# Performance work log

Hardware: AMD Instinct MI355X
Metric: run time of the kernel (lower is better)

Reference implementation:

```python
import jax, jax.numpy as jnp
import numpy as np

LEAN_TAU = 0.25
LEAN_DELTA = 0.35
O_ID = 0
NUM_LABELS = 9
HIDDEN = 1024


def setup_inputs() -> dict:
    key = jax.random.key(0)
    k = jax.random.split(key, 7)
    B, T = 64, 512
    hidden_states = jax.random.normal(k[0], (B, T, HIDDEN), dtype=jnp.float32)
    attention_mask = jnp.ones((B, T), dtype=jnp.int32)
    labels = jax.random.randint(k[1], (B, T), 0, NUM_LABELS).astype(jnp.int64)
    emis_w = jax.random.normal(k[2], (NUM_LABELS, HIDDEN), dtype=jnp.float32) * 0.02
    emis_b = jnp.zeros((NUM_LABELS,), dtype=jnp.float32)
    start_trans = jax.random.uniform(k[3], (NUM_LABELS,), minval=-0.1, maxval=0.1)
    end_trans = jax.random.uniform(k[4], (NUM_LABELS,), minval=-0.1, maxval=0.1)
    trans = jax.random.uniform(k[5], (NUM_LABELS, NUM_LABELS), minval=-0.1, maxval=0.1)
    return {
        "hidden_states": hidden_states,
        "emis_w": emis_w,
        "emis_b": emis_b,
        "start_trans": start_trans,
        "end_trans": end_trans,
        "trans": trans,
        "attention_mask": attention_mask,
        "labels": labels,
    }


def _crf_nll(logits, tags, mask, start_trans, end_trans, trans):
    """torchcrf CRF(batch_first=True), reduction='mean': -mean(log p(tags | logits))."""
    # time-major: [T, B, ...]
    e = jnp.swapaxes(logits, 0, 1)              # [T, B, L]
    tg = jnp.swapaxes(tags, 0, 1)               # [T, B]
    mk = jnp.swapaxes(mask, 0, 1).astype(logits.dtype)  # [T, B]
    B = e.shape[1]
    bidx = jnp.arange(B)

    # ----- numerator: score of gold path -----
    score0 = start_trans[tg[0]] + e[0, bidx, tg[0]]      # [B]
    last0 = tg[0]

    def num_step(carry, xs):
        score, last = carry
        e_t, t_t, t_prev, m_t = xs
        score = score + (trans[t_prev, t_t] + e_t[bidx, t_t]) * m_t
        last = jnp.where(m_t.astype(bool), t_t, last)
        return (score, last), None

    (num, last), _ = jax.lax.scan(num_step, (score0, last0),
                                  (e[1:], tg[1:], tg[:-1], mk[1:]))
    num = num + end_trans[last]

    # ----- denominator: partition via forward algorithm -----
    alpha0 = start_trans[None, :] + e[0]                 # [B, L]

    def den_step(alpha, xs):
        e_t, m_t = xs
        # alpha[b, i] + trans[i, j] + e_t[b, j] -> logsumexp over i
        nxt = jax.nn.logsumexp(alpha[:, :, None] + trans[None, :, :] + e_t[:, None, :], axis=1)
        alpha = jnp.where(m_t[:, None].astype(bool), nxt, alpha)
        return alpha, None

    alpha, _ = jax.lax.scan(den_step, alpha0, (e[1:], mk[1:]))
    den = jax.nn.logsumexp(alpha + end_trans[None, :], axis=1)  # [B]

    llh = num - den
    return -jnp.mean(llh)


def reference(hidden_states, emis_w, emis_b, start_trans, end_trans, trans,
              attention_mask, labels):
    # emission head
    logits = jnp.einsum('bth,lh->btl', hidden_states, emis_w) + emis_b  # [B, T, L]
    # strip special tokens ([CLS]/[SEP] positions)
    logits = logits[:, 1:-1, :]
    tok_mask = attention_mask[:, 1:-1].astype(bool)

    # lean-to-O on uncertain positions (torch.no_grad -> stop_gradient)
    det = jax.lax.stop_gradient(logits)
    top2 = jax.lax.top_k(det, 2)[0]                      # [B, T-2, 2]
    uncertain = ((top2[..., 0] - top2[..., 1]) < LEAN_TAU) & tok_mask
    logits = logits.at[..., O_ID].add(uncertain.astype(logits.dtype) * LEAN_DELTA)

    gold = labels[:, 1:-1]
    tags = jnp.where(gold == -100, 0, gold)
    mask = gold != -100
    return _crf_nll(logits, tags, mask, start_trans, end_trans, trans)
```

## Files before the change

### kernel.cpp

```cpp
#include <hip/hip_runtime.h>
#include <math.h>

#define HIDDEN 1024
#define NL 9
#define LEAN_TAU 0.25f
#define LEAN_DELTA 0.35f
#define LCH 16
#define TFIX 512
#define TOKFIX 510

typedef __attribute__((ext_vector_type(8))) short short8v;
typedef __attribute__((ext_vector_type(4))) float f32x4;
typedef __attribute__((ext_vector_type(4))) unsigned uint4v;
union frag_u { uint4v u; short8v s; };

__device__ __forceinline__ unsigned pk2(float a, float b) {
  return (__float_as_uint(b) & 0xffff0000u) | (__float_as_uint(a) >> 16);
}

__global__ __launch_bounds__(256) void mfma_k(
    const float* __restrict__ hs, const float* __restrict__ w,
    const float* __restrict__ bias, const int* __restrict__ amask,
    float* __restrict__ e, int B) {
  const int nTok = B * TOKFIX;
  const int wave = threadIdx.x >> 6, lane = threadIdx.x & 63;
  const int g = lane >> 4, c = lane & 15;
  __shared__ unsigned short aw[4][16][264];
  __shared__ float4 cp[3][64];

  const int base = blockIdx.x * 16;
  {
    int b = base / TOKFIX, t = base - b * TOKFIX;
#pragma unroll
    for (int j = 0; j < 16; ++j) {
      const int tok = base + j;
      const float* src =
          hs + ((size_t)b * TFIX + ((tok < nTok) ? t : 0) + 1) * HIDDEN;
      const float4 f =
          *reinterpret_cast<const float4*>(src + wave * 256 + lane * 4);
      uint2 pk;
      pk.x = pk2(f.x, f.y);
      pk.y = pk2(f.z, f.w);
      *reinterpret_cast<uint2*>(&aw[wave][j][lane * 4]) = pk;
      if (++t >= TOKFIX) { t = 0; ++b; }
    }
  }
  frag_u bfrag[8];
  {
    const int brow = (c < NL) ? c : 0;
    const float* wp = w + (size_t)brow * HIDDEN + wave * 256 + g * 8;
#pragma unroll
    for (int s = 0; s < 8; ++s) {
      const float4 u0 = *reinterpret_cast<const float4*>(wp + s * 32);
      const float4 u1 = *reinterpret_cast<const float4*>(wp + s * 32 + 4);
      unsigned d0 = pk2(u0.x, u0.y), d1 = pk2(u0.z, u0.w);
      unsigned d2 = pk2(u1.x, u1.y), d3 = pk2(u1.z, u1.w);
      if (c >= NL) d0 = d1 = d2 = d3 = 0u;
      bfrag[s].u = uint4v{d0, d1, d2, d3};
    }
  }
  __syncthreads();

  f32x4 acc = {0.f, 0.f, 0.f, 0.f};
#pragma unroll
  for (int s = 0; s < 8; ++s) {
    const short8v a =
        *reinterpret_cast<const short8v*>(&aw[wave][c][s * 32 + g * 8]);
    acc = __builtin_amdgcn_mfma_f32_16x16x32_bf16(a, bfrag[s].s, acc, 0, 0, 0);
  }

  if (wave != 0) cp[wave - 1][lane] = *reinterpret_cast<float4*>(&acc);
  __syncthreads();
  if (wave == 0) {
#pragma unroll
    for (int k = 0; k < 3; ++k) {
      const float4 p = cp[k][lane];
      acc[0] += p.x; acc[1] += p.y; acc[2] += p.z; acc[3] += p.w;
    }
    const float bc = (c < NL) ? bias[c] : 0.f;
#pragma unroll
    for (int j = 0; j < 4; ++j) {
      const int tok = base + g * 4 + j;
      const int tokc = (tok < nTok) ? tok : 0;
      const int b = tokc / TOKFIX, t = tokc - b * TOKFIX;
      const float v = acc[j] + bc;
      float m1 = (c < NL) ? v : -1e30f, m2 = -1e30f;
#pragma unroll
      for (int off = 1; off < 16; off <<= 1) {
        const float om1 = __shfl_xor(m1, off);
        const float om2 = __shfl_xor(m2, off);
        const float hi = fmaxf(m1, om1);
        const float lo = fminf(m1, om1);
        m2 = fmaxf(lo, fmaxf(m2, om2));
        m1 = hi;
      }
      const bool unc = (m1 - m2 < LEAN_TAU) && (amask[b * TFIX + t + 1] != 0);
      const float vout = v + ((unc && c == 0) ? LEAN_DELTA : 0.f);
      if (c < NL && tok < nTok) e[(size_t)tok * NL + c] = vout;
    }
  }
}

__global__ __launch_bounds__(64) void chunk_k(
    const float* __restrict__ e, const int* __restrict__ labels,
    const float* __restrict__ trans, float* __restrict__ Pout,
    int B, int T, int C) {
  const int TOK = T - 2;
  __shared__ float e2[7][LCH][NL];
  __shared__ float tr2[NL * NL];
  __shared__ int msk[7][LCH];
  const int tid = threadIdx.x;
  const int nG = B * C;
  const int gbase = blockIdx.x * 7;

  for (int idx = tid; idx < NL * NL; idx += 64) tr2[idx] = trans[idx];
  for (int idx = tid; idx < 7 * LCH * NL; idx += 64) {
    const int sub = idx / (LCH * NL), rem = idx % (LCH * NL);
    const int step = rem / NL, j = rem % NL;
    const int g = gbase + sub;
    if (g < nG) {
      const int b = g / C, c = g % C;
      const int t = 1 + c * LCH + step;
      if (t < TOK) e2[sub][step][j] = e[((size_t)b * TOK + t) * NL + j];
    }
  }
  for (int idx = tid; idx < 7 * LCH; idx += 64) {
    const int sub = idx / LCH, step = idx % LCH;
    const int g = gbase + sub;
    if (g < nG) {
      const int b = g / C, c = g % C;
      const int t = 1 + c * LCH + step;
      msk[sub][step] = (t < TOK) ? (labels[(size_t)b * T + 1 + t] != -100) : 0;
    }
  }
  __syncthreads();

  const int sub = tid / NL, i = tid % NL;
  const int g = gbase + sub;
  const bool act = (sub < 7) && (g < nG);
  int len = 1;
  if (act) { const int c = g % C; len = min(LCH, TOK - (1 + c * LCH)); }

  float W[NL][NL];
#pragma unroll
  for (int k = 0; k < NL; ++k)
#pragma unroll
    for (int j = 0; j < NL; ++j) W[k][j] = __expf(tr2[k * NL + j]);

  float P[NL];
  {
    const int m0 = act ? msk[sub][0] : 0;
#pragma unroll
    for (int j = 0; j < NL; ++j)
      P[j] = m0 ? (tr2[i * NL + j] + e2[sub][0][j])
                : ((i == j) ? 0.f : -1e30f);
  }
  for (int step = 1; step < len; ++step) {
    const int mt = msk[sub][step];
    float mx = P[0];
#pragma unroll
    for (int k = 1; k < NL; ++k) mx = fmaxf(mx, P[k]);
    float E[NL];
#pragma unroll
    for (int k = 0; k < NL; ++k) E[k] = __expf(P[k] - mx);
    float Pn[NL];
#pragma unroll
    for (int j = 0; j < NL; ++j) {
      float s = 0.f;
#pragma unroll
      for (int k = 0; k < NL; ++k) s = fmaf(E[k], W[k][j], s);
      Pn[j] = mx + __logf(s) + e2[sub][step][j];
    }
#pragma unroll
    for (int j = 0; j < NL; ++j) P[j] = mt ? Pn[j] : P[j];
  }
  if (act) {
    float* dst = Pout + (size_t)g * 81 + i * NL;
#pragma unroll
    for (int j = 0; j < NL; ++j) dst[j] = P[j];
  }
}

__global__ __launch_bounds__(64) void combine_k(
    const float* __restrict__ e, const int* __restrict__ labels,
    const float* __restrict__ start_t, const float* __restrict__ end_t,
    const float* __restrict__ trans, const float* __restrict__ Pmat,
    float* __restrict__ llh, int B, int T, int C) {
  const int TOK = T - 2;
  const int b = blockIdx.x, lane = threadIdx.x;
  const float* eb = e + (size_t)b * TOK * NL;
  const int* lb = labels + (size_t)b * T + 1;

  const int g0r = lb[0];
  const int tg0 = (g0r == -100) ? 0 : g0r;
  float nsum = 0.f;
  int pack = -1;
  for (int t = 1 + lane; t < TOK; t += 64) {
    const int gr = lb[t], pr = lb[t - 1];
    if (gr != -100) {
      const int cur = gr;
      const int prev = (pr == -100) ? 0 : pr;
      nsum += trans[prev * NL + cur] + eb[t * NL + cur];
      pack = (t << 4) | cur;
    }
  }
#pragma unroll
  for (int off = 32; off; off >>= 1) {
    nsum += __shfl_xor(nsum, off);
    pack = max(pack, __shfl_xor(pack, off));
  }
  const int last = (pack < 0) ? tg0 : (pack & 15);
  const float num = start_t[tg0] + eb[tg0] + nsum + end_t[last];

  float alpha = (lane < NL) ? (start_t[lane] + eb[lane]) : -1e30f;
  for (int c = 0; c < C; ++c) {
    const float* Pc = Pmat + ((size_t)b * C + c) * 81;
    float col[NL];
#pragma unroll
    for (int i = 0; i < NL; ++i)
      col[i] = (lane < NL) ? Pc[i * NL + lane] : -1e30f;
    float s[NL];
    float mx = -1e30f;
#pragma unroll
    for (int i = 0; i < NL; ++i) {
      const float ai = __shfl(alpha, i);
      s[i] = ai + col[i];
      mx = fmaxf(mx, s[i]);
    }
    float sum = 0.f;
#pragma unroll
    for (int i = 0; i < NL; ++i) sum += __expf(s[i] - mx);
    const float nx = mx + __logf(sum);
    alpha = (lane < NL) ? nx : -1e30f;
  }
  const float v = (lane < NL) ? (alpha + end_t[lane]) : -1e30f;
  float mx = v;
#pragma unroll
  for (int off = 32; off; off >>= 1) mx = fmaxf(mx, __shfl_xor(mx, off));
  float sum = (lane < NL) ? __expf(v - mx) : 0.f;
#pragma unroll
  for (int off = 32; off; off >>= 1) sum += __shfl_xor(sum, off);
  const float den = mx + __logf(sum);
  if (lane == 0) llh[b] = num - den;
}

__global__ __launch_bounds__(64) void reduce_k(const float* __restrict__ llh,
                                               float* __restrict__ out, int B) {
  float v = 0.f;
  for (int i = threadIdx.x; i < B; i += 64) v += llh[i];
#pragma unroll
  for (int off = 32; off; off >>= 1) v += __shfl_xor(v, off);
  if (threadIdx.x == 0) out[0] = -v / (float)B;
}

extern "C" void kernel_launch(void* const* d_in, const int* in_sizes, int n_in,
                              void* d_out, int out_size, void* d_ws,
                              size_t ws_size, hipStream_t stream) {
  const float* hs     = (const float*)d_in[0];
  const float* w      = (const float*)d_in[1];
  const float* bias   = (const float*)d_in[2];
  const float* st     = (const float*)d_in[3];
  const float* et     = (const float*)d_in[4];
  const float* tr     = (const float*)d_in[5];
  const int*   amask  = (const int*)d_in[6];
  const int*   labels = (const int*)d_in[7];

  const int T = 512;
  const int B = in_sizes[6] / T;
  const int TOK = T - 2;
  const int C = (TOK - 1 + LCH - 1) / LCH;

  float* e    = (float*)d_ws;
  float* llh  = e + (size_t)B * TOK * NL;
  float* Pmat = llh + B;

  const int nTok = B * TOK;
  const int nTile = (nTok + 15) / 16;
  mfma_k<<<nTile, 256, 0, stream>>>(hs, w, bias, amask, e, B);
  const int nG = B * C;
  chunk_k<<<(nG + 6) / 7, 64, 0, stream>>>(e, labels, tr, Pmat, B, T, C);
  combine_k<<<B, 64, 0, stream>>>(e, labels, st, et, tr, Pmat, llh, B, T, C);
  reduce_k<<<1, 64, 0, stream>>>(llh, (float*)d_out, B);
}
```

Baseline: 73.36 us.

## Make emission MFMA kernel persistent with register-prefetched next tile

The emission GEMM kernel now runs as a persistent grid of at most 680 blocks that loop over 16-token tiles. Each block keeps the weight fragments in registers across tiles, loads the next tile's hidden states into registers while computing the current one, and shares the epilogue across all four waves instead of leaving it to wave 0. The aim is to overlap global loads with MFMA work and to cut per-block setup and idle waves on this memory-bound stage. In exchange it uses 16 extra float4 registers per thread, which can lower occupancy. The last-tile padding guard is removed, so correctness relies on the token count dividing evenly by 16.

After: 77.27 us. +5.3%, slower.

```diff
diff --git a/kernel.cpp b/kernel.cpp
--- a/kernel.cpp
+++ b/kernel.cpp
@@ -23,28 +23,12 @@
     const float* __restrict__ bias, const int* __restrict__ amask,
     float* __restrict__ e, int B) {
   const int nTok = B * TOKFIX;
+  const int nTile = nTok >> 4;
   const int wave = threadIdx.x >> 6, lane = threadIdx.x & 63;
   const int g = lane >> 4, c = lane & 15;
   __shared__ unsigned short aw[4][16][264];
-  __shared__ float4 cp[3][64];
-
-  const int base = blockIdx.x * 16;
-  {
-    int b = base / TOKFIX, t = base - b * TOKFIX;
-#pragma unroll
-    for (int j = 0; j < 16; ++j) {
-      const int tok = base + j;
-      const float* src =
-          hs + ((size_t)b * TFIX + ((tok < nTok) ? t : 0) + 1) * HIDDEN;
-      const float4 f =
-          *reinterpret_cast<const float4*>(src + wave * 256 + lane * 4);
-      uint2 pk;
-      pk.x = pk2(f.x, f.y);
-      pk.y = pk2(f.z, f.w);
-      *reinterpret_cast<uint2*>(&aw[wave][j][lane * 4]) = pk;
-      if (++t >= TOKFIX) { t = 0; ++b; }
-    }
-  }
+  __shared__ float4 cps[4][64];
+
   frag_u bfrag[8];
   {
     const int brow = (c < NL) ? c : 0;
@@ -59,31 +43,56 @@
       bfrag[s].u = uint4v{d0, d1, d2, d3};
     }
   }
+  const float bc = (c < NL) ? bias[c] : 0.f;
+
+  float4 st[16];
+
+#define LOADTILE(TT)                                                        \
+  {                                                                         \
+    int b_ = ((TT)*16) / TOKFIX, t_ = ((TT)*16) - b_ * TOKFIX;              \
+    _Pragma("unroll") for (int j_ = 0; j_ < 16; ++j_) {                     \
+      st[j_] = *reinterpret_cast<const float4*>(                            \
+          hs + ((size_t)b_ * TFIX + t_ + 1) * HIDDEN + wave * 256 +         \
+          lane * 4);                                                        \
+      if (++t_ >= TOKFIX) { t_ = 0; ++b_; }                                 \
+    }                                                                       \
+  }
+#define PACKWRITE()                                                         \
+  {                                                                         \
+    _Pragma("unroll") for (int j_ = 0; j_ < 16; ++j_) {                     \
+      uint2 pk_;                                                            \
+      pk_.x = pk2(st[j_].x, st[j_].y);                                      \
+      pk_.y = pk2(st[j_].z, st[j_].w);                                      \
+      *reinterpret_cast<uint2*>(&aw[wave][j_][lane * 4]) = pk_;             \
+    }                                                                       \
+  }
+
+  int tile = blockIdx.x;
+  if (tile >= nTile) return;
+  LOADTILE(tile);
+  PACKWRITE();
   __syncthreads();
 
-  f32x4 acc = {0.f, 0.f, 0.f, 0.f};
-#pragma unroll
-  for (int s = 0; s < 8; ++s) {
-    const short8v a =
-        *reinterpret_cast<const short8v*>(&aw[wave][c][s * 32 + g * 8]);
-    acc = __builtin_amdgcn_mfma_f32_16x16x32_bf16(a, bfrag[s].s, acc, 0, 0, 0);
-  }
-
-  if (wave != 0) cp[wave - 1][lane] = *reinterpret_cast<float4*>(&acc);
-  __syncthreads();
-  if (wave == 0) {
-#pragma unroll
-    for (int k = 0; k < 3; ++k) {
-      const float4 p = cp[k][lane];
-      acc[0] += p.x; acc[1] += p.y; acc[2] += p.z; acc[3] += p.w;
-    }
-    const float bc = (c < NL) ? bias[c] : 0.f;
-#pragma unroll
-    for (int j = 0; j < 4; ++j) {
-      const int tok = base + g * 4 + j;
-      const int tokc = (tok < nTok) ? tok : 0;
-      const int b = tokc / TOKFIX, t = tokc - b * TOKFIX;
-      const float v = acc[j] + bc;
+  while (true) {
+    const int tileN = tile + gridDim.x;
+    const bool hasN = tileN < nTile;
+    if (hasN) LOADTILE(tileN);
+
+    f32x4 acc = {0.f, 0.f, 0.f, 0.f};
+#pragma unroll
+    for (int s = 0; s < 8; ++s) {
+      const short8v a =
+          *reinterpret_cast<const short8v*>(&aw[wave][c][s * 32 + g * 8]);
+      acc = __builtin_amdgcn_mfma_f32_16x16x32_bf16(a, bfrag[s].s, acc, 0, 0, 0);
+    }
+    cps[wave][lane] = *reinterpret_cast<float4*>(&acc);
+    __syncthreads();
+
+    {
+      float v = bc;
+#pragma unroll
+      for (int k = 0; k < 4; ++k)
+        v += reinterpret_cast<const float*>(&cps[k][lane])[wave];
       float m1 = (c < NL) ? v : -1e30f, m2 = -1e30f;
 #pragma unroll
       for (int off = 1; off < 16; off <<= 1) {
@@ -94,11 +103,19 @@
         m2 = fmaxf(lo, fmaxf(m2, om2));
         m1 = hi;
       }
+      const int tok = tile * 16 + g * 4 + wave;
+      const int b = tok / TOKFIX, t = tok - b * TOKFIX;
       const bool unc = (m1 - m2 < LEAN_TAU) && (amask[b * TFIX + t + 1] != 0);
       const float vout = v + ((unc && c == 0) ? LEAN_DELTA : 0.f);
       if (c < NL && tok < nTok) e[(size_t)tok * NL + c] = vout;
     }
-  }
+    if (hasN) PACKWRITE();
+    __syncthreads();
+    if (!hasN) break;
+    tile = tileN;
+  }
+#undef LOADTILE
+#undef PACKWRITE
 }
 
 __global__ __launch_bounds__(64) void chunk_k(
@@ -276,7 +293,9 @@
 
   const int nTok = B * TOK;
   const int nTile = (nTok + 15) / 16;
-  mfma_k<<<nTile, 256, 0, stream>>>(hs, w, bias, amask, e, B);
+  int grid1 = 680;
+  if (grid1 > nTile) grid1 = nTile;
+  mfma_k<<<grid1, 256, 0, stream>>>(hs, w, bias, amask, e, B);
   const int nG = B * C;
   chunk_k<<<(nG + 6) / 7, 64, 0, stream>>>(e, labels, tr, Pmat, B, T, C);
   combine_k<<<B, 64, 0, stream>>>(e, labels, st, et, tr, Pmat, llh, B, T, C);
```

## Fuse CRF chunk scan and combine into one per-sequence block kernel

Applied to the files above, without the earlier changes.

Merges the chunked transfer-matrix kernel and the combine kernel into one kernel with one 512-thread block per sequence. Emissions and labels for the sequence are staged in shared memory, the 32 chunk matrices stay in shared memory, and the numerator and the alpha combine run in separate waves. This removes a kernel launch and the global round trip of the chunk matrices, but each block does a serial combine and uses only 64 blocks on the GPU.

Measured after the change: 60.41 us (median of 2 runs). 17.7% less time.

```diff
diff --git a/kernel.cpp b/kernel.cpp
--- a/kernel.cpp
+++ b/kernel.cpp
@@ -101,147 +101,124 @@
   }
 }
 
-__global__ __launch_bounds__(64) void chunk_k(
+__global__ __launch_bounds__(512) void crf_k(
     const float* __restrict__ e, const int* __restrict__ labels,
-    const float* __restrict__ trans, float* __restrict__ Pout,
+    const float* __restrict__ start_t, const float* __restrict__ end_t,
+    const float* __restrict__ trans, float* __restrict__ llh,
     int B, int T, int C) {
   const int TOK = T - 2;
-  __shared__ float e2[7][LCH][NL];
-  __shared__ float tr2[NL * NL];
-  __shared__ int msk[7][LCH];
+  const int NSTEP = TOK - 1;
+  const int b = blockIdx.x;
   const int tid = threadIdx.x;
-  const int nG = B * C;
-  const int gbase = blockIdx.x * 7;
-
-  for (int idx = tid; idx < NL * NL; idx += 64) tr2[idx] = trans[idx];
-  for (int idx = tid; idx < 7 * LCH * NL; idx += 64) {
-    const int sub = idx / (LCH * NL), rem = idx % (LCH * NL);
-    const int step = rem / NL, j = rem % NL;
-    const int g = gbase + sub;
-    if (g < nG) {
-      const int b = g / C, c = g % C;
-      const int t = 1 + c * LCH + step;
-      if (t < TOK) e2[sub][step][j] = e[((size_t)b * TOK + t) * NL + j];
-    }
-  }
-  for (int idx = tid; idx < 7 * LCH; idx += 64) {
-    const int sub = idx / LCH, step = idx % LCH;
-    const int g = gbase + sub;
-    if (g < nG) {
-      const int b = g / C, c = g % C;
-      const int t = 1 + c * LCH + step;
-      msk[sub][step] = (t < TOK) ? (labels[(size_t)b * T + 1 + t] != -100) : 0;
-    }
-  }
-  __syncthreads();
-
-  const int sub = tid / NL, i = tid % NL;
-  const int g = gbase + sub;
-  const bool act = (sub < 7) && (g < nG);
-  int len = 1;
-  if (act) { const int c = g % C; len = min(LCH, TOK - (1 + c * LCH)); }
-
-  float W[NL][NL];
-#pragma unroll
-  for (int k = 0; k < NL; ++k)
-#pragma unroll
-    for (int j = 0; j < NL; ++j) W[k][j] = __expf(tr2[k * NL + j]);
-
-  float P[NL];
-  {
-    const int m0 = act ? msk[sub][0] : 0;
-#pragma unroll
-    for (int j = 0; j < NL; ++j)
-      P[j] = m0 ? (tr2[i * NL + j] + e2[sub][0][j])
-                : ((i == j) ? 0.f : -1e30f);
-  }
-  for (int step = 1; step < len; ++step) {
-    const int mt = msk[sub][step];
-    float mx = P[0];
-#pragma unroll
-    for (int k = 1; k < NL; ++k) mx = fmaxf(mx, P[k]);
-    float E[NL];
-#pragma unroll
-    for (int k = 0; k < NL; ++k) E[k] = __expf(P[k] - mx);
-    float Pn[NL];
-#pragma unroll
-    for (int j = 0; j < NL; ++j) {
-      float s = 0.f;
-#pragma unroll
-      for (int k = 0; k < NL; ++k) s = fmaf(E[k], W[k][j], s);
-      Pn[j] = mx + __logf(s) + e2[sub][step][j];
-    }
-#pragma unroll
-    for (int j = 0; j < NL; ++j) P[j] = mt ? Pn[j] : P[j];
-  }
-  if (act) {
-    float* dst = Pout + (size_t)g * 81 + i * NL;
-#pragma unroll
-    for (int j = 0; j < NL; ++j) dst[j] = P[j];
-  }
-}
-
-__global__ __launch_bounds__(64) void combine_k(
-    const float* __restrict__ e, const int* __restrict__ labels,
-    const float* __restrict__ start_t, const float* __restrict__ end_t,
-    const float* __restrict__ trans, const float* __restrict__ Pmat,
-    float* __restrict__ llh, int B, int T, int C) {
-  const int TOK = T - 2;
-  const int b = blockIdx.x, lane = threadIdx.x;
+  const int wave = tid >> 6, lane = tid & 63;
+
+  __shared__ float esh[TOKFIX * NL];
+  __shared__ float Psh[32][NL * NL + 3];
+  __shared__ int lsh[TOKFIX];
+  __shared__ float numsh;
+
   const float* eb = e + (size_t)b * TOK * NL;
-  const int* lb = labels + (size_t)b * T + 1;
-
-  const int g0r = lb[0];
-  const int tg0 = (g0r == -100) ? 0 : g0r;
-  float nsum = 0.f;
-  int pack = -1;
-  for (int t = 1 + lane; t < TOK; t += 64) {
-    const int gr = lb[t], pr = lb[t - 1];
-    if (gr != -100) {
-      const int cur = gr;
-      const int prev = (pr == -100) ? 0 : pr;
-      nsum += trans[prev * NL + cur] + eb[t * NL + cur];
-      pack = (t << 4) | cur;
-    }
-  }
-#pragma unroll
-  for (int off = 32; off; off >>= 1) {
-    nsum += __shfl_xor(nsum, off);
-    pack = max(pack, __shfl_xor(pack, off));
-  }
-  const int last = (pack < 0) ? tg0 : (pack & 15);
-  const float num = start_t[tg0] + eb[tg0] + nsum + end_t[last];
-
-  float alpha = (lane < NL) ? (start_t[lane] + eb[lane]) : -1e30f;
-  for (int c = 0; c < C; ++c) {
-    const float* Pc = Pmat + ((size_t)b * C + c) * 81;
-    float col[NL];
-#pragma unroll
-    for (int i = 0; i < NL; ++i)
-      col[i] = (lane < NL) ? Pc[i * NL + lane] : -1e30f;
-    float s[NL];
-    float mx = -1e30f;
-#pragma unroll
-    for (int i = 0; i < NL; ++i) {
-      const float ai = __shfl(alpha, i);
-      s[i] = ai + col[i];
-      mx = fmaxf(mx, s[i]);
-    }
-    float sum = 0.f;
-#pragma unroll
-    for (int i = 0; i < NL; ++i) sum += __expf(s[i] - mx);
-    const float nx = mx + __logf(sum);
-    alpha = (lane < NL) ? nx : -1e30f;
-  }
-  const float v = (lane < NL) ? (alpha + end_t[lane]) : -1e30f;
-  float mx = v;
-#pragma unroll
-  for (int off = 32; off; off >>= 1) mx = fmaxf(mx, __shfl_xor(mx, off));
-  float sum = (lane < NL) ? __expf(v - mx) : 0.f;
-#pragma unroll
-  for (int off = 32; off; off >>= 1) sum += __shfl_xor(sum, off);
-  const float den = mx + __logf(sum);
-  if (lane == 0) llh[b] = num - den;
+  for (int i = tid; i < TOK * NL; i += 512) esh[i] = eb[i];
+  for (int i = tid; i < TOK; i += 512) lsh[i] = labels[(size_t)b * T + 1 + i];
+  __syncthreads();
+
+  const int sub = lane / 9, i9 = lane - sub * 9;
+  const int c = wave * 7 + sub;
+  if (sub < 7 && c < C) {
+    float W[NL][NL];
+#pragma unroll
+    for (int k = 0; k < NL; ++k)
+#pragma unroll
+      for (int j = 0; j < NL; ++j) W[k][j] = __expf(trans[k * NL + j]);
+    int len = NSTEP - c * LCH;
+    if (len > LCH) len = LCH;
+    const int t0 = 1 + c * LCH;
+    float P[NL];
+    {
+      const int m0 = (lsh[t0] != -100);
+#pragma unroll
+      for (int j = 0; j < NL; ++j)
+        P[j] = m0 ? (trans[i9 * NL + j] + esh[t0 * NL + j])
+                  : ((i9 == j) ? 0.f : -1e30f);
+    }
+    for (int s = 1; s < len; ++s) {
+      const int mt = (lsh[t0 + s] != -100);
+      float mx = P[0];
+#pragma unroll
+      for (int k = 1; k < NL; ++k) mx = fmaxf(mx, P[k]);
+      float E[NL];
+#pragma unroll
+      for (int k = 0; k < NL; ++k) E[k] = __expf(P[k] - mx);
+      float Pn[NL];
+#pragma unroll
+      for (int j = 0; j < NL; ++j) {
+        float sm = 0.f;
+#pragma unroll
+        for (int k = 0; k < NL; ++k) sm = fmaf(E[k], W[k][j], sm);
+        Pn[j] = mx + __logf(sm) + esh[(t0 + s) * NL + j];
+      }
+#pragma unroll
+      for (int j = 0; j < NL; ++j) P[j] = mt ? Pn[j] : P[j];
+    }
+#pragma unroll
+    for (int j = 0; j < NL; ++j) Psh[c][i9 * NL + j] = P[j];
+  }
+  __syncthreads();
+
+  if (wave == 1) {
+    const int g0r = lsh[0];
+    const int tg0 = (g0r == -100) ? 0 : g0r;
+    float nsum = 0.f;
+    int pack = -1;
+    for (int t = 1 + lane; t < TOK; t += 64) {
+      const int gr = lsh[t], pr = lsh[t - 1];
+      if (gr != -100) {
+        const int prev = (pr == -100) ? 0 : pr;
+        nsum += trans[prev * NL + gr] + esh[t * NL + gr];
+        pack = (t << 4) | gr;
+      }
+    }
+#pragma unroll
+    for (int off = 32; off; off >>= 1) {
+      nsum += __shfl_xor(nsum, off);
+      pack = max(pack, __shfl_xor(pack, off));
+    }
+    const int last = (pack < 0) ? tg0 : (pack & 15);
+    if (lane == 0)
+      numsh = start_t[tg0] + esh[tg0] + nsum + end_t[last];
+  }
+  float den = 0.f;
+  if (wave == 0) {
+    float alpha = (lane < NL) ? (start_t[lane] + esh[lane]) : -1e30f;
+    for (int cc = 0; cc < C; ++cc) {
+      float col[NL];
+#pragma unroll
+      for (int i = 0; i < NL; ++i)
+        col[i] = (lane < NL) ? Psh[cc][i * NL + lane] : -1e30f;
+      float s[NL], mx = -1e30f;
+#pragma unroll
+      for (int i = 0; i < NL; ++i) {
+        const float ai = __shfl(alpha, i);
+        s[i] = ai + col[i];
+        mx = fmaxf(mx, s[i]);
+      }
+      float sum = 0.f;
+#pragma unroll
+      for (int i = 0; i < NL; ++i) sum += __expf(s[i] - mx);
+      const float nx = mx + __logf(sum);
+      alpha = (lane < NL) ? nx : -1e30f;
+    }
+    const float v = (lane < NL) ? (alpha + end_t[lane]) : -1e30f;
+    float mx = v;
+#pragma unroll
+    for (int off = 32; off; off >>= 1) mx = fmaxf(mx, __shfl_xor(mx, off));
+    float sum = (lane < NL) ? __expf(v - mx) : 0.f;
+#pragma unroll
+    for (int off = 32; off; off >>= 1) sum += __shfl_xor(sum, off);
+    den = mx + __logf(sum);
+  }
+  __syncthreads();
+  if (wave == 0 && lane == 0) llh[b] = numsh - den;
 }
 
 __global__ __launch_bounds__(64) void reduce_k(const float* __restrict__ llh,
@@ -270,15 +247,12 @@
   const int TOK = T - 2;
   const int C = (TOK - 1 + LCH - 1) / LCH;
 
-  float* e    = (float*)d_ws;
-  float* llh  = e + (size_t)B * TOK * NL;
-  float* Pmat = llh + B;
+  float* e   = (float*)d_ws;
+  float* llh = e + (size_t)B * TOK * NL;
 
   const int nTok = B * TOK;
   const int nTile = (nTok + 15) / 16;
   mfma_k<<<nTile, 256, 0, stream>>>(hs, w, bias, amask, e, B);
-  const int nG = B * C;
-  chunk_k<<<(nG + 6) / 7, 64, 0, stream>>>(e, labels, tr, Pmat, B, T, C);
-  combine_k<<<B, 64, 0, stream>>>(e, labels, st, et, tr, Pmat, llh, B, T, C);
+  crf_k<<<B, 512, 0, stream>>>(e, labels, st, et, tr, llh, B, T, C);
   reduce_k<<<1, 64, 0, stream>>>(llh, (float*)d_out, B);
 }
```
